# Optimization experiments

Hardware: AMD Instinct MI355X
Metric: run time of the kernel (lower is better)

The kernel has to match this reference:

```python
import jax, jax.numpy as jnp
import numpy as np

T, B, H = 1024, 256, 20


def setup_inputs() -> dict:
    key = jax.random.key(0)
    ks = jax.random.split(key, 6)

    def lin_w(k, fan_in, fan_out):
        bound = 1.0 / np.sqrt(fan_in)
        return jax.random.uniform(k, (fan_in, fan_out), jnp.float32, -bound, bound)

    # t is time-reversed (torch.flip): strictly decreasing, so dt = t[0]-t[1] > 0
    t = jnp.linspace(1.0, 0.0, T, dtype=jnp.float32).reshape(T, 1)
    y = jax.random.uniform(ks[0], (B, 1, 3), jnp.float32)  # initial SIR state per batch
    return {
        "t": t,
        "y": y,
        "w1": lin_w(ks[1], 1, H), "b1": jnp.zeros((H,), jnp.float32),
        "w2": lin_w(ks[2], H, H), "b2": jnp.zeros((H,), jnp.float32),
        "w3": lin_w(ks[3], H, H), "b3": jnp.zeros((H,), jnp.float32),
        "w4": lin_w(ks[4], H, 1), "b4": jnp.zeros((1,), jnp.float32),
        "beta": jnp.asarray(0.2, jnp.float32),
        "gamma": jnp.asarray(0.2, jnp.float32),
    }


def reference(t, y, w1, b1, w2, b2, w3, b3, w4, b4, beta, gamma):
    Tn = t.shape[0]
    dt = t[0, 0] - t[1, 0]  # positive scalar (t is reversed)

    # memory kernel me(t): Linear-Tanh x3 -> Linear-Sigmoid, shape [T]
    h = jnp.tanh(t @ w1 + b1)
    h = jnp.tanh(h @ w2 + b2)
    h = jnp.tanh(h @ w3 + b3)
    me = jax.nn.sigmoid(h @ w4 + b4)[:, 0]  # [T]
    # pad so me[-j:] can be read as a fixed-length dynamic slice (zeros past end)
    me_pad = jnp.concatenate([me, jnp.zeros((Tn,), me.dtype)])  # [2T]

    y0 = jnp.transpose(y, (1, 0, 2))[0]  # [B,3]  (y.transpose(1,0) then first/only row)
    Bn = y0.shape[0]
    # history buffer of I-compartment values; entries >= current length stay zero
    I_hist0 = jnp.zeros((Tn, Bn), y0.dtype).at[0].set(y0[:, 1])

    def step(carry, idx):
        y_cur, I_hist = carry  # y_cur [B,3], I_hist [T,B]
        j = idx + 1  # current solution length
        # kernel slice w[k] = me[T - j + k]; for k >= j both w (padding) and I_hist are 0
        w = jax.lax.dynamic_slice(me_pad, (Tn - j,), (Tn,))  # [T]
        integ = dt * jnp.einsum('t,tb->b', w, I_hist)  # memory integral, [B]
        S, I = y_cur[:, 0], y_cur[:, 1]
        bSI = beta * S * I
        gI = gamma * I
        d = jnp.stack([-bSI + integ, bSI - gI, gI - integ], axis=1)  # [B,3]
        y_next = y_cur + d * dt  # forward Euler
        I_hist = I_hist.at[j].set(y_next[:, 1])
        return (y_next, I_hist), (d, y_next)

    (_, _), (ds, ys) = jax.lax.scan(step, (y0, I_hist0), jnp.arange(Tn - 1))
    solution = jnp.concatenate([y0[None], ys], axis=0)  # [T,B,3]
    # original leaves diff[T-1] as zeros (loop fills rows 0..T-2)
    diff = jnp.concatenate([ds, jnp.zeros((1, Bn, 3), ds.dtype)], axis=0)  # [T,B,3]
    return solution, diff
```

## Files before the change

kernel.cpp:

```cpp
#include <hip/hip_runtime.h>

#define T_N 1024
#define B_N 256
#define H_N 20
#define NW  8
#define NDW (NW - 1)
#define SIH 1096

typedef _Float16 h8_t __attribute__((ext_vector_type(8)));

#if __has_builtin(__builtin_amdgcn_fdot2)
#define DOT8(acc, mv, iv)                                                           \
    acc = __builtin_amdgcn_fdot2(__builtin_shufflevector(mv, mv, 0, 1),             \
                                 __builtin_shufflevector(iv, iv, 0, 1), acc, false);\
    acc = __builtin_amdgcn_fdot2(__builtin_shufflevector(mv, mv, 2, 3),             \
                                 __builtin_shufflevector(iv, iv, 2, 3), acc, false);\
    acc = __builtin_amdgcn_fdot2(__builtin_shufflevector(mv, mv, 4, 5),             \
                                 __builtin_shufflevector(iv, iv, 4, 5), acc, false);\
    acc = __builtin_amdgcn_fdot2(__builtin_shufflevector(mv, mv, 6, 7),             \
                                 __builtin_shufflevector(iv, iv, 6, 7), acc, false);
#else
#define DOT8(acc, mv, iv)                                                           \
    _Pragma("unroll")                                                               \
    for (int _k = 0; _k < 8; ++_k) acc = fmaf((float)mv[_k], (float)iv[_k], acc);
#endif

__device__ __forceinline__ float rdlane_i(float v, int lane) {
    return __uint_as_float((unsigned)__builtin_amdgcn_readlane((int)__float_as_uint(v), lane));
}
__device__ __forceinline__ float fast_tanh(float x) {
    const float e = __expf(2.0f * x);
    return fmaf(-2.0f, __builtin_amdgcn_rcpf(e + 1.0f), 1.0f);
}
__device__ __forceinline__ float fast_sigmoid(float x) {
    return __builtin_amdgcn_rcpf(1.0f + __expf(-x));
}

#define REP64(F) \
    F(0) F(1) F(2) F(3) F(4) F(5) F(6) F(7) F(8) F(9) F(10) F(11) F(12) F(13) \
    F(14) F(15) F(16) F(17) F(18) F(19) F(20) F(21) F(22) F(23) F(24) F(25)   \
    F(26) F(27) F(28) F(29) F(30) F(31) F(32) F(33) F(34) F(35) F(36) F(37)   \
    F(38) F(39) F(40) F(41) F(42) F(43) F(44) F(45) F(46) F(47) F(48) F(49)   \
    F(50) F(51) F(52) F(53) F(54) F(55) F(56) F(57) F(58) F(59) F(60) F(61)   \
    F(62) F(63)

__global__ __launch_bounds__(512, 1) void scan_kernel(
    const float* __restrict__ t,
    const float* __restrict__ y,
    const float* __restrict__ w1, const float* __restrict__ b1,
    const float* __restrict__ w2, const float* __restrict__ b2,
    const float* __restrict__ w3, const float* __restrict__ b3,
    const float* __restrict__ w4, const float* __restrict__ b4,
    const float* __restrict__ beta_p,
    const float* __restrict__ gamma_p,
    float* __restrict__ out)
{
    __shared__ __align__(16) float    sMeF[T_N];
    __shared__ __align__(16) _Float16 sMeH[T_N];
    __shared__ __align__(16) _Float16 sIhR[8 * SIH];
    __shared__ __align__(16) float    P[2][64][8];

    const int b   = blockIdx.x;
    const int tid = threadIdx.x;
    const int wid = tid >> 6;
    const int L   = tid & 63;

    const int f    = (-L) & 7;
    const int R8   = L + f;
    const int row  = L & 7;
    const int iofs = row * SIH + (f ? 0 : 8);

    if (tid < 64) sIhR[(tid >> 3) * SIH + (tid & 7)] = (_Float16)0.0f;
    if (tid < 128) P[tid >> 6][tid & 63][7] = 0.0f;

#pragma unroll
    for (int v = 0; v < 2; ++v) {
        const int mi = tid + v * 512;
        const float x = t[mi];

        float h1[H_N], h2[H_N];
#pragma unroll
        for (int k = 0; k < H_N; ++k) h1[k] = fast_tanh(fmaf(x, w1[k], b1[k]));

#pragma unroll 4
        for (int k = 0; k < H_N; ++k) {
            float a = b2[k];
#pragma unroll
            for (int j = 0; j < H_N; ++j) a = fmaf(h1[j], w2[j * H_N + k], a);
            h2[k] = fast_tanh(a);
        }

        float a4 = b4[0];
#pragma unroll 4
        for (int k = 0; k < H_N; ++k) {
            float a = b3[k];
#pragma unroll
            for (int j = 0; j < H_N; ++j) a = fmaf(h2[j], w3[j * H_N + k], a);
            a4 = fmaf(fast_tanh(a), w4[k], a4);
        }

        const float meval = fast_sigmoid(a4);
        sMeF[mi] = meval;
        sMeH[mi] = (_Float16)meval;
    }

    const float dt    = t[0] - t[1];
    const float beta  = beta_p[0];
    const float gma   = gamma_p[0];
    const float invdt = 1.0f / dt;
    const float dt2   = dt * dt;

    const float S0 = y[b * 3 + 0];
    const float I0 = y[b * 3 + 1];
    const float R0 = y[b * 3 + 2];
    const float TOT = S0 + I0 + R0;

    if (tid < 8) sIhR[tid * SIH + 8 - tid] = (_Float16)I0;

    float* __restrict__ diff = out + (size_t)T_N * B_N * 3;
    if (tid < 3) diff[((size_t)(T_N - 1) * B_N + b) * 3 + tid] = 0.0f;

    __syncthreads();

    float mf[7];
#pragma unroll
    for (int d = 1; d <= 7; ++d) mf[d - 1] = sMeF[T_N - 64 - L - d];

    const float dtb   = dt * beta;
    const float ndtb  = -dtb;
    const float c1    = fmaf(-dt, gma, 1.0f);
    const float meT1s = dt2 * sMeF[T_N - 1];

    float S = S0, I = I0, oS = S0, oI = I0;
    float acc_cur = 0.0f, acc_nxt = 0.0f, pre = 0.0f;
    float carryS = S0, carryI = I0;

#define TBLDECL(k) float rm_##k, rn_##k;
    REP64(TBLDECL)
#undef TBLDECL
    if (wid == 0) {
#define TBLINIT(k)                                                          \
        rm_##k = (((k) < L) ? sMeF[T_N - L + (k)] : 0.0f) * dt2;            \
        rn_##k = dt2 * sMeF[T_N - 64 - L + (k)];
        REP64(TBLINIT)
#undef TBLINIT
#define TBLPIN(k) asm volatile("" : "+v"(rm_##k), "+v"(rn_##k));
        REP64(TBLPIN)
#undef TBLPIN
        __builtin_amdgcn_s_setprio(3);
    }

#define STEPB(M_, FIRST_)                                               \
    {                                                                   \
        const float sum = (FIRST_) ? pre : fmaf(meT1s, I, pre);         \
        float pnx = pre;                                                \
        if ((M_) < 63) pnx = rdlane_i(acc_cur, (M_) + 1);               \
        const float a  = fmaf(dtb, S, c1);                              \
        const float bb = fmaf(ndtb, I, 1.0f);                           \
        S = fmaf(bb, S, sum);                                           \
        I = I * a;                                                      \
        const bool cap = (L == (M_));                                   \
        oS = cap ? S : oS;                                              \
        oI = cap ? I : oI;                                              \
        acc_cur = fmaf(rm_##M_, I, acc_cur);                            \
        acc_nxt = fmaf(rn_##M_, I, acc_nxt);                            \
        pre = pnx;                                                      \
    }
#define STEP_GE1(M_) if ((M_) >= 1) STEPB(M_, false)
#define STEP_GE2(M_) if ((M_) >= 2) STEPB(M_, false)

    for (int c = 0; c < 16; ++c) {
        if (wid == 0) {
            if (c == 0) {
                acc_cur = rm_0 * I;
                acc_nxt = rn_0 * I;
                pre = rdlane_i(acc_cur, 1);
                STEPB(1, true)
                REP64(STEP_GE2)
            } else {
                const float4 pa = *(const float4*)&P[c & 1][L][0];
                const float4 pb = *(const float4*)&P[c & 1][L][4];
                const float ps = ((pa.x + pa.y) + (pa.z + pa.w)) +
                                 ((pb.x + pb.y) + (pb.z + pb.w));
                acc_cur = fmaf(dt2, ps, acc_nxt);
                acc_nxt = 0.0f;
                pre = rdlane_i(acc_cur, 0);
                STEPB(0, true)
                REP64(STEP_GE1)
            }

            const int j = 64 * c + L;
            const _Float16 hI = (_Float16)oI;
#pragma unroll
            for (int r = 0; r < 8; ++r) sIhR[r * SIH + 8 + (j - r)] = hI;

            const float oR = TOT - oS - oI;
            const size_t so = ((size_t)j * B_N + b) * 3;
            out[so + 0] = oS;
            out[so + 1] = oI;
            out[so + 2] = oR;

            float sm1 = __shfl_up(oS, 1);
            float im1 = __shfl_up(oI, 1);
            if (L == 0) { sm1 = carryS; im1 = carryI; }
            if (j > 0) {
                const float d0 = (oS - sm1) * invdt;
                const float d1 = (oI - im1) * invdt;
                const float d2 = -d0 - d1;
                const size_t dofs = ((size_t)(j - 1) * B_N + b) * 3;
                diff[dofs + 0] = d0;
                diff[dofs + 1] = d1;
                diff[dofs + 2] = d2;
            }
            carryS = rdlane_i(oS, 63);
            carryI = rdlane_i(oI, 63);
        } else if (c < 15) {
            const int w    = wid - 1;
            const int G    = 8 * c;
            const int idx0 = (T_N - 64 * (c + 1)) - R8;
            float p0 = 0.0f, p1 = 0.0f;
            int s = w;
            for (; s + NDW < G; s += 2 * NDW) {
                const h8_t mv0 = *(const h8_t*)&sMeH[idx0 + 8 * s];
                const h8_t iv0 = *(const h8_t*)&sIhR[iofs + 8 * s];
                const h8_t mv1 = *(const h8_t*)&sMeH[idx0 + 8 * (s + NDW)];
                const h8_t iv1 = *(const h8_t*)&sIhR[iofs + 8 * (s + NDW)];
                DOT8(p0, mv0, iv0)
                DOT8(p1, mv1, iv1)
            }
            if (s < G) {
                const h8_t mv0 = *(const h8_t*)&sMeH[idx0 + 8 * s];
                const h8_t iv0 = *(const h8_t*)&sIhR[iofs + 8 * s];
                DOT8(p0, mv0, iv0)
            }
            float p = p0 + p1;
            if (w == 0) {
#pragma unroll
                for (int d = 1; d <= 7; ++d) {
                    const float ih = (float)sIhR[8 + 64 * c - d];
                    if (d <= f) p = fmaf(mf[d - 1], ih, p);
                }
            }
            P[(c + 1) & 1][L][w] = p;
        }
        __syncthreads();
    }
#undef STEPB
#undef STEP_GE1
#undef STEP_GE2
}

extern "C" void kernel_launch(void* const* d_in, const int* in_sizes, int n_in,
                              void* d_out, int out_size, void* d_ws, size_t ws_size,
                              hipStream_t stream) {
    const float* t     = (const float*)d_in[0];
    const float* y     = (const float*)d_in[1];
    const float* w1    = (const float*)d_in[2];
    const float* b1    = (const float*)d_in[3];
    const float* w2    = (const float*)d_in[4];
    const float* b2    = (const float*)d_in[5];
    const float* w3    = (const float*)d_in[6];
    const float* b3    = (const float*)d_in[7];
    const float* w4    = (const float*)d_in[8];
    const float* b4    = (const float*)d_in[9];
    const float* beta  = (const float*)d_in[10];
    const float* gamma = (const float*)d_in[11];

    scan_kernel<<<B_N, 512, 0, stream>>>(t, y, w1, b1, w2, b2, w3, b3, w4, b4,
                                         beta, gamma, (float*)d_out);
}
```

Before: 119.3 us.

## Hoist memory-kernel MLP into separate kernel computed once via workspace

Previously each of the 256 blocks recomputed the whole 1024-point MLP memory kernel redundantly. This moves that computation into a small two-block pre-kernel that writes fp32 and fp16 results to the workspace, and the scan kernel now only loads them into shared memory. The partial-sum buffer P is also split into two separate arrays, PA and PB. The trade is an extra kernel launch and a global round-trip in exchange for removing the redundant per-block MLP work from the scan kernel's prologue.

```diff
diff --git a/kernel.cpp b/kernel.cpp
--- a/kernel.cpp
+++ b/kernel.cpp
@@ -44,13 +44,49 @@
     F(50) F(51) F(52) F(53) F(54) F(55) F(56) F(57) F(58) F(59) F(60) F(61)   \
     F(62) F(63)
 
-__global__ __launch_bounds__(512, 1) void scan_kernel(
+__global__ __launch_bounds__(512, 1) void me_kernel(
     const float* __restrict__ t,
-    const float* __restrict__ y,
     const float* __restrict__ w1, const float* __restrict__ b1,
     const float* __restrict__ w2, const float* __restrict__ b2,
     const float* __restrict__ w3, const float* __restrict__ b3,
     const float* __restrict__ w4, const float* __restrict__ b4,
+    float* __restrict__ me_f,
+    _Float16* __restrict__ me_h)
+{
+    const int gid = blockIdx.x * 512 + threadIdx.x;
+    const float x = t[gid];
+
+    float h1[H_N], h2[H_N];
+#pragma unroll
+    for (int k = 0; k < H_N; ++k) h1[k] = fast_tanh(fmaf(x, w1[k], b1[k]));
+
+#pragma unroll 4
+    for (int k = 0; k < H_N; ++k) {
+        float a = b2[k];
+#pragma unroll
+        for (int j = 0; j < H_N; ++j) a = fmaf(h1[j], w2[j * H_N + k], a);
+        h2[k] = fast_tanh(a);
+    }
+
+    float a4 = b4[0];
+#pragma unroll 4
+    for (int k = 0; k < H_N; ++k) {
+        float a = b3[k];
+#pragma unroll
+        for (int j = 0; j < H_N; ++j) a = fmaf(h2[j], w3[j * H_N + k], a);
+        a4 = fmaf(fast_tanh(a), w4[k], a4);
+    }
+
+    const float meval = fast_sigmoid(a4);
+    me_f[gid] = meval;
+    me_h[gid] = (_Float16)meval;
+}
+
+__global__ __launch_bounds__(512, 1) void scan_kernel(
+    const float* __restrict__ me_f,
+    const _Float16* __restrict__ me_h,
+    const float* __restrict__ t,
+    const float* __restrict__ y,
     const float* __restrict__ beta_p,
     const float* __restrict__ gamma_p,
     float* __restrict__ out)
@@ -58,7 +94,8 @@
     __shared__ __align__(16) float    sMeF[T_N];
     __shared__ __align__(16) _Float16 sMeH[T_N];
     __shared__ __align__(16) _Float16 sIhR[8 * SIH];
-    __shared__ __align__(16) float    P[2][64][8];
+    __shared__ __align__(16) float    PA[2][64][4];
+    __shared__ __align__(16) float    PB[2][64][4];
 
     const int b   = blockIdx.x;
     const int tid = threadIdx.x;
@@ -71,37 +108,13 @@
     const int iofs = row * SIH + (f ? 0 : 8);
 
     if (tid < 64) sIhR[(tid >> 3) * SIH + (tid & 7)] = (_Float16)0.0f;
-    if (tid < 128) P[tid >> 6][tid & 63][7] = 0.0f;
+    if (tid < 128) PB[tid >> 6][tid & 63][3] = 0.0f;
 
 #pragma unroll
     for (int v = 0; v < 2; ++v) {
         const int mi = tid + v * 512;
-        const float x = t[mi];
-
-        float h1[H_N], h2[H_N];
-#pragma unroll
-        for (int k = 0; k < H_N; ++k) h1[k] = fast_tanh(fmaf(x, w1[k], b1[k]));
-
-#pragma unroll 4
-        for (int k = 0; k < H_N; ++k) {
-            float a = b2[k];
-#pragma unroll
-            for (int j = 0; j < H_N; ++j) a = fmaf(h1[j], w2[j * H_N + k], a);
-            h2[k] = fast_tanh(a);
-        }
-
-        float a4 = b4[0];
-#pragma unroll 4
-        for (int k = 0; k < H_N; ++k) {
-            float a = b3[k];
-#pragma unroll
-            for (int j = 0; j < H_N; ++j) a = fmaf(h2[j], w3[j * H_N + k], a);
-            a4 = fmaf(fast_tanh(a), w4[k], a4);
-        }
-
-        const float meval = fast_sigmoid(a4);
-        sMeF[mi] = meval;
-        sMeH[mi] = (_Float16)meval;
+        sMeF[mi] = me_f[mi];
+        sMeH[mi] = me_h[mi];
     }
 
     const float dt    = t[0] - t[1];
@@ -178,8 +191,8 @@
                 STEPB(1, true)
                 REP64(STEP_GE2)
             } else {
-                const float4 pa = *(const float4*)&P[c & 1][L][0];
-                const float4 pb = *(const float4*)&P[c & 1][L][4];
+                const float4 pa = *(const float4*)&PA[c & 1][L][0];
+                const float4 pb = *(const float4*)&PB[c & 1][L][0];
                 const float ps = ((pa.x + pa.y) + (pa.z + pa.w)) +
                                  ((pb.x + pb.y) + (pb.z + pb.w));
                 acc_cur = fmaf(dt2, ps, acc_nxt);
@@ -241,7 +254,8 @@
                     if (d <= f) p = fmaf(mf[d - 1], ih, p);
                 }
             }
-            P[(c + 1) & 1][L][w] = p;
+            if (w < 4) PA[(c + 1) & 1][L][w] = p;
+            else       PB[(c + 1) & 1][L][w - 4] = p;
         }
         __syncthreads();
     }
@@ -266,6 +280,9 @@
     const float* beta  = (const float*)d_in[10];
     const float* gamma = (const float*)d_in[11];
 
-    scan_kernel<<<B_N, 512, 0, stream>>>(t, y, w1, b1, w2, b2, w3, b3, w4, b4,
-                                         beta, gamma, (float*)d_out);
-}
+    float*    me_f = (float*)d_ws;
+    _Float16* me_h = (_Float16*)((char*)d_ws + 4096);
+
+    me_kernel<<<2, 512, 0, stream>>>(t, w1, b1, w2, b2, w3, b3, w4, b4, me_f, me_h);
+    scan_kernel<<<B_N, 512, 0, stream>>>(me_f, me_h, t, y, beta, gamma, (float*)d_out);
+}
```

New measurement: 114.2 us. 4.3% less time.
